# Performance work log

Measured on AMD Instinct MI355X. Metric: run time of the kernel, lower is better.

## Reference

```python
import jax, jax.numpy as jnp
import numpy as np

S, DIM, E, K = 16384, 4096, 64, 2

def setup_inputs() -> dict:
    key = jax.random.key(0)
    kx, kw = jax.random.split(key)
    x = jax.random.normal(kx, (S, DIM), dtype=jnp.float32)
    W = jax.random.normal(kw, (E, DIM), dtype=jnp.float32) * (1.0 / np.sqrt(DIM))
    b = jnp.zeros((E,), dtype=jnp.float32)
    return {"x": x, "W": W, "b": b}

def reference(x, W, b):
    # Router linear: [S, dim] @ [dim, E] + [E] -> [S, E]
    logits = jnp.einsum('sd,ed->se', x, W) + b
    probs = jax.nn.softmax(logits, axis=-1)              # [S, E]
    topk_vals, topk_idx = jax.lax.top_k(probs, K)        # [S, K], [S, K]
    # Load-balance aux loss (Switch Transformer style)
    importance = probs.mean(axis=0)                      # [E]
    hard1 = topk_idx[:, 0]                               # [S]
    load = jax.ops.segment_sum(jnp.ones((S,), dtype=probs.dtype), hard1,
                               num_segments=E) / max(S, 1)
    aux_loss = E * jnp.sum(importance * load)
    return (topk_idx, topk_vals, aux_loss)
```

## Files before the change

### kernel.cpp

```cpp
#include <hip/hip_runtime.h>
#include <hip/hip_bf16.h>

#define SROWS 16384
#define DIMK  4096
#define NE    64
#define BM    16
#define NBLK  (SROWS/BM)
#define NSTEP 16
#define WSPLIT_SHORTS 262144
#define WSOFF_F 262144
#define WSOFF2  (WSOFF_F + NBLK*64)

typedef __attribute__((ext_vector_type(8))) short short8;
typedef __attribute__((ext_vector_type(4))) float f32x4;

__device__ __forceinline__ void split8(const float4 a, const float4 c, short8& hi, short8& lo) {
    float f[8] = {a.x, a.y, a.z, a.w, c.x, c.y, c.z, c.w};
    #pragma unroll
    for (int i = 0; i < 8; ++i) {
        unsigned short h = __bfloat16_as_ushort(__float2bfloat16(f[i]));
        float hf = __uint_as_float((unsigned)h << 16);
        unsigned short l = __bfloat16_as_ushort(__float2bfloat16(f[i] - hf));
        hi[i] = (short)h;
        lo[i] = (short)l;
    }
}

__global__ void w_split(const float* __restrict__ W, unsigned short* __restrict__ wsp)
{
    const int idx   = blockIdx.x * 256 + threadIdx.x;
    const int kslot = idx & 511;
    const int e     = idx >> 9;
    const float* p = W + (size_t)e * DIMK + kslot * 8;
    float4 va = *reinterpret_cast<const float4*>(p);
    float4 vb = *reinterpret_cast<const float4*>(p + 4);
    short8 hi, lo;
    split8(va, vb, hi, lo);
    *reinterpret_cast<short8*>(wsp + (size_t)(kslot * 64 + e) * 8)                 = hi;
    *reinterpret_cast<short8*>(wsp + WSPLIT_SHORTS + (size_t)(kslot * 64 + e) * 8) = lo;
}

__device__ __forceinline__ void gl_lds16(const void* g, void* l) {
    __builtin_amdgcn_global_load_lds(
        (const __attribute__((address_space(1))) void*)g,
        (__attribute__((address_space(3))) void*)l, 16, 0, 0);
}

__global__ __launch_bounds__(256, 4) void gate_main(
    const float* __restrict__ x, const unsigned short* __restrict__ wsp,
    const float* __restrict__ b, float* __restrict__ out, float* __restrict__ ws)
{
    __shared__ __align__(16) char smem[32768];

    const int tid  = threadIdx.x;
    const int lane = tid & 63;
    const int ksw  = __builtin_amdgcn_readfirstlane(tid >> 6);
    const int row0 = blockIdx.x * BM;

    const float* xsq[4];
    #pragma unroll
    for (int q = 0; q < 4; ++q) {
        const int r = ksw * 4 + q;
        xsq[q] = x + (size_t)(row0 + r) * DIMK + ((lane ^ (r & 7)) * 4);
    }

    auto STAGE = [&](int st, int bsel) {
        char* xb = smem + bsel * 16384;
        #pragma unroll
        for (int q = 0; q < 4; ++q)
            gl_lds16(xsq[q] + (size_t)st * 256, xb + (ksw * 4 + q) * 1024 + lane * 16);
    };

    f32x4 acc[4];
    #pragma unroll
    for (int n = 0; n < 4; ++n) acc[n] = (f32x4){0.f, 0.f, 0.f, 0.f};

    const int rm = lane & 7;
    const char* xrow = smem + (lane & 15) * 1024;

    STAGE(0, 0);

    #pragma unroll 1
    for (int st = 0; st < NSTEP; ++st) {
        asm volatile("s_waitcnt vmcnt(0)" ::: "memory");
        __builtin_amdgcn_s_barrier();
        __builtin_amdgcn_sched_barrier(0);
        if (st + 1 < NSTEP) STAGE(st + 1, (st + 1) & 1);

        const char* xb = xrow + (st & 1) * 16384;

        #pragma unroll
        for (int c2 = 0; c2 < 2; ++c2) {
            const int ga = ksw * 16 + c2 * 8 + 2 * (lane >> 4);
            float4 xa = *reinterpret_cast<const float4*>(xb + ((ga    ) ^ rm) * 16);
            float4 xc = *reinterpret_cast<const float4*>(xb + ((ga + 1) ^ rm) * 16);
            short8 ah, al;
            split8(xa, xc, ah, al);

            const int ksl = st * 32 + ksw * 8 + c2 * 4 + (lane >> 4);
            const unsigned short* bp = wsp + ((size_t)ksl * 64 + (lane & 15)) * 8;
            short8 bh[4], bl[4];
            #pragma unroll
            for (int n = 0; n < 4; ++n) {
                bh[n] = *reinterpret_cast<const short8*>(bp + n * 128);
                bl[n] = *reinterpret_cast<const short8*>(bp + WSPLIT_SHORTS + n * 128);
            }

            #pragma unroll
            for (int n = 0; n < 4; ++n)
                acc[n] = __builtin_amdgcn_mfma_f32_16x16x32_bf16(ah, bh[n], acc[n], 0, 0, 0);
            #pragma unroll
            for (int n = 0; n < 4; ++n)
                acc[n] = __builtin_amdgcn_mfma_f32_16x16x32_bf16(ah, bl[n], acc[n], 0, 0, 0);
            #pragma unroll
            for (int n = 0; n < 4; ++n)
                acc[n] = __builtin_amdgcn_mfma_f32_16x16x32_bf16(al, bh[n], acc[n], 0, 0, 0);
        }
    }

    __syncthreads();

    float* const part = reinterpret_cast<float*>(smem);
    float* const Lb   = reinterpret_cast<float*>(smem + 12288);
    float* const red  = reinterpret_cast<float*>(smem + 17792);

    if (ksw > 0) {
        #pragma unroll
        for (int n = 0; n < 4; ++n)
            #pragma unroll
            for (int j = 0; j < 4; ++j)
                part[(ksw - 1) * 1024 + lane * 16 + n * 4 + j] = acc[n][j];
    }
    __syncthreads();
    if (ksw == 0) {
        #pragma unroll
        for (int n = 0; n < 4; ++n) {
            #pragma unroll
            for (int j = 0; j < 4; ++j) {
                float v = acc[n][j]
                        + part[0 * 1024 + lane * 16 + n * 4 + j]
                        + part[1 * 1024 + lane * 16 + n * 4 + j]
                        + part[2 * 1024 + lane * 16 + n * 4 + j];
                const int e  = n * 16 + (lane & 15);
                const int rl = (lane >> 4) * 4 + j;
                Lb[e * 17 + rl] = v;
            }
        }
    }
    __syncthreads();

    float impAcc = 0.f, cntAcc = 0.f;
    const float blane = b[lane];
    float* outIdx = out;
    float* outVal = out + (size_t)SROWS * 2;

    #pragma unroll 1
    for (int rr = 0; rr < 4; ++rr) {
        const int r = ksw * 4 + rr;
        const float logit = Lb[lane * 17 + r] + blane;

        float v1 = logit; int i1 = lane;
        #pragma unroll
        for (int off = 32; off; off >>= 1) {
            float ov = __shfl_xor(v1, off);
            int   oi = __shfl_xor(i1, off);
            if (ov > v1 || (ov == v1 && oi < i1)) { v1 = ov; i1 = oi; }
        }
        float p = expf(logit - v1);
        float ssum = p;
        #pragma unroll
        for (int off = 32; off; off >>= 1) ssum += __shfl_xor(ssum, off);

        float v2 = (lane == i1) ? -3.402823466e38f : logit;
        int i2 = lane;
        #pragma unroll
        for (int off = 32; off; off >>= 1) {
            float ov = __shfl_xor(v2, off);
            int   oi = __shfl_xor(i2, off);
            if (ov > v2 || (ov == v2 && oi < i2)) { v2 = ov; i2 = oi; }
        }

        impAcc += p / ssum;
        cntAcc += (i1 == lane) ? 1.f : 0.f;

        if (lane == 0) {
            const int sr = row0 + r;
            outIdx[sr * 2 + 0] = (float)i1;
            outIdx[sr * 2 + 1] = (float)i2;
            outVal[sr * 2 + 0] = 1.f / ssum;
            outVal[sr * 2 + 1] = expf(v2 - v1) / ssum;
        }
    }

    __syncthreads();
    red[ksw * 64 + lane]       = impAcc;
    red[256 + ksw * 64 + lane] = cntAcc;
    __syncthreads();
    if (tid < 64) {
        float si = 0.f, sc2 = 0.f;
        #pragma unroll
        for (int g = 0; g < 4; ++g) {
            si  += red[g * 64 + tid];
            sc2 += red[256 + g * 64 + tid];
        }
        ws[WSOFF_F + (size_t)blockIdx.x * 64 + tid] = si;
        ws[WSOFF2  + (size_t)blockIdx.x * 64 + tid] = sc2;
    }
}

__global__ void gate_reduce(const float* __restrict__ ws, float* __restrict__ out)
{
    __shared__ float li[64 * 64], lc[64 * 64];
    const int t = threadIdx.x;
    const int g  = t >> 4;
    const int e4 = (t & 15) * 4;
    float4 si = make_float4(0.f, 0.f, 0.f, 0.f);
    float4 sc = make_float4(0.f, 0.f, 0.f, 0.f);
    const int base = g * 16;
    #pragma unroll 4
    for (int bb = base; bb < base + 16; ++bb) {
        float4 a = *reinterpret_cast<const float4*>(&ws[WSOFF_F + (size_t)bb * 64 + e4]);
        float4 c = *reinterpret_cast<const float4*>(&ws[WSOFF2  + (size_t)bb * 64 + e4]);
        si.x += a.x; si.y += a.y; si.z += a.z; si.w += a.w;
        sc.x += c.x; sc.y += c.y; sc.z += c.z; sc.w += c.w;
    }
    *reinterpret_cast<float4*>(&li[g * 64 + e4]) = si;
    *reinterpret_cast<float4*>(&lc[g * 64 + e4]) = sc;
    __syncthreads();
    if (t < 64) {
        float ti = 0.f, tc = 0.f;
        #pragma unroll 8
        for (int gg = 0; gg < 64; ++gg) { ti += li[gg * 64 + t]; tc += lc[gg * 64 + t]; }
        li[t] = ti * tc;
    }
    __syncthreads();
    if (t == 0) {
        float s = 0.f;
        for (int i = 0; i < NE; ++i) s += li[i];
        out[(size_t)SROWS * 4] = s * ((float)NE / ((float)SROWS * (float)SROWS));
    }
}

extern "C" void kernel_launch(void* const* d_in, const int* in_sizes, int n_in,
                              void* d_out, int out_size, void* d_ws, size_t ws_size,
                              hipStream_t stream)
{
    const float* x = (const float*)d_in[0];
    const float* W = (const float*)d_in[1];
    const float* b = (const float*)d_in[2];
    float* out = (float*)d_out;
    unsigned short* wsp = (unsigned short*)d_ws;
    float* wsf = (float*)d_ws;

    w_split<<<128, 256, 0, stream>>>(W, wsp);
    gate_main<<<NBLK, 256, 0, stream>>>(x, wsp, b, out, wsf);
    gate_reduce<<<1, 1024, 0, stream>>>(wsf, out);
}
```

Before: 89.47 us.

## Use 16 waves per block with wider split-K and dynamic LDS

```diff
diff --git a/kernel.cpp b/kernel.cpp
--- a/kernel.cpp
+++ b/kernel.cpp
@@ -6,10 +6,11 @@
 #define NE    64
 #define BM    16
 #define NBLK  (SROWS/BM)
-#define NSTEP 16
+#define NSTEP 8
 #define WSPLIT_SHORTS 262144
 #define WSOFF_F 262144
 #define WSOFF2  (WSOFF_F + NBLK*64)
+#define LDS_BYTES 98304
 
 typedef __attribute__((ext_vector_type(8))) short short8;
 typedef __attribute__((ext_vector_type(4))) float f32x4;
@@ -46,29 +47,24 @@
         (__attribute__((address_space(3))) void*)l, 16, 0, 0);
 }
 
-__global__ __launch_bounds__(256, 4) void gate_main(
+__global__ __launch_bounds__(1024, 4) void gate_main(
     const float* __restrict__ x, const unsigned short* __restrict__ wsp,
     const float* __restrict__ b, float* __restrict__ out, float* __restrict__ ws)
 {
-    __shared__ __align__(16) char smem[32768];
+    extern __shared__ __align__(16) char smem[];
 
     const int tid  = threadIdx.x;
     const int lane = tid & 63;
-    const int ksw  = __builtin_amdgcn_readfirstlane(tid >> 6);
+    const int wid  = __builtin_amdgcn_readfirstlane(tid >> 6);
     const int row0 = blockIdx.x * BM;
 
-    const float* xsq[4];
-    #pragma unroll
-    for (int q = 0; q < 4; ++q) {
-        const int r = ksw * 4 + q;
-        xsq[q] = x + (size_t)(row0 + r) * DIMK + ((lane ^ (r & 7)) * 4);
-    }
+    const float* xs0 = x + (size_t)(row0 + wid) * DIMK + (lane ^ (wid & 7)) * 4;
+    const float* xs1 = xs0 + 256;
 
     auto STAGE = [&](int st, int bsel) {
-        char* xb = smem + bsel * 16384;
-        #pragma unroll
-        for (int q = 0; q < 4; ++q)
-            gl_lds16(xsq[q] + (size_t)st * 256, xb + (ksw * 4 + q) * 1024 + lane * 16);
+        char* xb = smem + bsel * 32768 + wid * 2048;
+        gl_lds16(xs0 + (size_t)st * 512, xb + lane * 16);
+        gl_lds16(xs1 + (size_t)st * 512, xb + 1024 + lane * 16);
     };
 
     f32x4 acc[4];
@@ -76,71 +72,72 @@
     for (int n = 0; n < 4; ++n) acc[n] = (f32x4){0.f, 0.f, 0.f, 0.f};
 
     const int rm = lane & 7;
-    const char* xrow = smem + (lane & 15) * 1024;
+    const char* xrow = smem + (lane & 15) * 2048;
+    const int ga = wid * 8 + 2 * (lane >> 4);
 
     STAGE(0, 0);
+    asm volatile("s_waitcnt vmcnt(0)" ::: "memory");
+    __builtin_amdgcn_s_barrier();
+    __builtin_amdgcn_sched_barrier(0);
 
     #pragma unroll 1
     for (int st = 0; st < NSTEP; ++st) {
+        if (st + 1 < NSTEP) STAGE(st + 1, (st + 1) & 1);
+        __builtin_amdgcn_sched_barrier(0);
+
+        const char* xb = xrow + (st & 1) * 32768;
+        float4 xa = *reinterpret_cast<const float4*>(xb + ((ga    ) ^ rm) * 16);
+        float4 xc = *reinterpret_cast<const float4*>(xb + ((ga + 1) ^ rm) * 16);
+        short8 ah, al;
+        split8(xa, xc, ah, al);
+
+        const int ksl = st * 64 + wid * 4 + (lane >> 4);
+        const unsigned short* bp = wsp + ((size_t)ksl * 64 + (lane & 15)) * 8;
+        short8 bh[4], bl[4];
+        #pragma unroll
+        for (int n = 0; n < 4; ++n) {
+            bh[n] = *reinterpret_cast<const short8*>(bp + n * 128);
+            bl[n] = *reinterpret_cast<const short8*>(bp + WSPLIT_SHORTS + n * 128);
+        }
+
+        #pragma unroll
+        for (int n = 0; n < 4; ++n)
+            acc[n] = __builtin_amdgcn_mfma_f32_16x16x32_bf16(ah, bh[n], acc[n], 0, 0, 0);
+        #pragma unroll
+        for (int n = 0; n < 4; ++n)
+            acc[n] = __builtin_amdgcn_mfma_f32_16x16x32_bf16(ah, bl[n], acc[n], 0, 0, 0);
+        #pragma unroll
+        for (int n = 0; n < 4; ++n)
+            acc[n] = __builtin_amdgcn_mfma_f32_16x16x32_bf16(al, bh[n], acc[n], 0, 0, 0);
+
         asm volatile("s_waitcnt vmcnt(0)" ::: "memory");
         __builtin_amdgcn_s_barrier();
         __builtin_amdgcn_sched_barrier(0);
-        if (st + 1 < NSTEP) STAGE(st + 1, (st + 1) & 1);
-
-        const char* xb = xrow + (st & 1) * 16384;
-
-        #pragma unroll
-        for (int c2 = 0; c2 < 2; ++c2) {
-            const int ga = ksw * 16 + c2 * 8 + 2 * (lane >> 4);
-            float4 xa = *reinterpret_cast<const float4*>(xb + ((ga    ) ^ rm) * 16);
-            float4 xc = *reinterpret_cast<const float4*>(xb + ((ga + 1) ^ rm) * 16);
-            short8 ah, al;
-            split8(xa, xc, ah, al);
-
-            const int ksl = st * 32 + ksw * 8 + c2 * 4 + (lane >> 4);
-            const unsigned short* bp = wsp + ((size_t)ksl * 64 + (lane & 15)) * 8;
-            short8 bh[4], bl[4];
-            #pragma unroll
-            for (int n = 0; n < 4; ++n) {
-                bh[n] = *reinterpret_cast<const short8*>(bp + n * 128);
-                bl[n] = *reinterpret_cast<const short8*>(bp + WSPLIT_SHORTS + n * 128);
-            }
-
-            #pragma unroll
-            for (int n = 0; n < 4; ++n)
-                acc[n] = __builtin_amdgcn_mfma_f32_16x16x32_bf16(ah, bh[n], acc[n], 0, 0, 0);
-            #pragma unroll
-            for (int n = 0; n < 4; ++n)
-                acc[n] = __builtin_amdgcn_mfma_f32_16x16x32_bf16(ah, bl[n], acc[n], 0, 0, 0);
-            #pragma unroll
-            for (int n = 0; n < 4; ++n)
-                acc[n] = __builtin_amdgcn_mfma_f32_16x16x32_bf16(al, bh[n], acc[n], 0, 0, 0);
-        }
     }
 
     __syncthreads();
 
     float* const part = reinterpret_cast<float*>(smem);
-    float* const Lb   = reinterpret_cast<float*>(smem + 12288);
-    float* const red  = reinterpret_cast<float*>(smem + 17792);
-
-    if (ksw > 0) {
+    float* const Lb   = reinterpret_cast<float*>(smem + 61440);
+    float* const red  = reinterpret_cast<float*>(smem + 65792);
+
+    if (wid > 0) {
         #pragma unroll
         for (int n = 0; n < 4; ++n)
             #pragma unroll
             for (int j = 0; j < 4; ++j)
-                part[(ksw - 1) * 1024 + lane * 16 + n * 4 + j] = acc[n][j];
-    }
-    __syncthreads();
-    if (ksw == 0) {
+                part[(wid - 1) * 1024 + lane * 16 + n * 4 + j] = acc[n][j];
+    }
+    __syncthreads();
+    if (wid == 0) {
         #pragma unroll
         for (int n = 0; n < 4; ++n) {
             #pragma unroll
             for (int j = 0; j < 4; ++j) {
-                float v = acc[n][j]
-                        + part[0 * 1024 + lane * 16 + n * 4 + j]
-                        + part[1 * 1024 + lane * 16 + n * 4 + j]
-                        + part[2 * 1024 + lane * 16 + n * 4 + j];
+                float v = acc[n][j];
+                #pragma unroll
+                for (int g = 0; g < 15; ++g)
+                    v += part[g * 1024 + lane * 16 + n * 4 + j];
                 const int e  = n * 16 + (lane & 15);
                 const int rl = (lane >> 4) * 4 + j;
                 Lb[e * 17 + rl] = v;
@@ -149,59 +146,55 @@
     }
     __syncthreads();
 
-    float impAcc = 0.f, cntAcc = 0.f;
     const float blane = b[lane];
     float* outIdx = out;
     float* outVal = out + (size_t)SROWS * 2;
 
-    #pragma unroll 1
-    for (int rr = 0; rr < 4; ++rr) {
-        const int r = ksw * 4 + rr;
-        const float logit = Lb[lane * 17 + r] + blane;
-
-        float v1 = logit; int i1 = lane;
-        #pragma unroll
-        for (int off = 32; off; off >>= 1) {
-            float ov = __shfl_xor(v1, off);
-            int   oi = __shfl_xor(i1, off);
-            if (ov > v1 || (ov == v1 && oi < i1)) { v1 = ov; i1 = oi; }
-        }
-        float p = expf(logit - v1);
-        float ssum = p;
-        #pragma unroll
-        for (int off = 32; off; off >>= 1) ssum += __shfl_xor(ssum, off);
-
-        float v2 = (lane == i1) ? -3.402823466e38f : logit;
-        int i2 = lane;
-        #pragma unroll
-        for (int off = 32; off; off >>= 1) {
-            float ov = __shfl_xor(v2, off);
-            int   oi = __shfl_xor(i2, off);
-            if (ov > v2 || (ov == v2 && oi < i2)) { v2 = ov; i2 = oi; }
-        }
-
-        impAcc += p / ssum;
-        cntAcc += (i1 == lane) ? 1.f : 0.f;
-
-        if (lane == 0) {
-            const int sr = row0 + r;
-            outIdx[sr * 2 + 0] = (float)i1;
-            outIdx[sr * 2 + 1] = (float)i2;
-            outVal[sr * 2 + 0] = 1.f / ssum;
-            outVal[sr * 2 + 1] = expf(v2 - v1) / ssum;
-        }
-    }
-
-    __syncthreads();
-    red[ksw * 64 + lane]       = impAcc;
-    red[256 + ksw * 64 + lane] = cntAcc;
+    const int r = wid;
+    const float logit = Lb[lane * 17 + r] + blane;
+
+    float v1 = logit; int i1 = lane;
+    #pragma unroll
+    for (int off = 32; off; off >>= 1) {
+        float ov = __shfl_xor(v1, off);
+        int   oi = __shfl_xor(i1, off);
+        if (ov > v1 || (ov == v1 && oi < i1)) { v1 = ov; i1 = oi; }
+    }
+    float p = expf(logit - v1);
+    float ssum = p;
+    #pragma unroll
+    for (int off = 32; off; off >>= 1) ssum += __shfl_xor(ssum, off);
+
+    float v2 = (lane == i1) ? -3.402823466e38f : logit;
+    int i2 = lane;
+    #pragma unroll
+    for (int off = 32; off; off >>= 1) {
+        float ov = __shfl_xor(v2, off);
+        int   oi = __shfl_xor(i2, off);
+        if (ov > v2 || (ov == v2 && oi < i2)) { v2 = ov; i2 = oi; }
+    }
+
+    const float impAcc = p / ssum;
+    const float cntAcc = (i1 == lane) ? 1.f : 0.f;
+
+    if (lane == 0) {
+        const int sr = row0 + r;
+        outIdx[sr * 2 + 0] = (float)i1;
+        outIdx[sr * 2 + 1] = (float)i2;
+        outVal[sr * 2 + 0] = 1.f / ssum;
+        outVal[sr * 2 + 1] = expf(v2 - v1) / ssum;
+    }
+
+    __syncthreads();
+    red[wid * 64 + lane]        = impAcc;
+    red[1024 + wid * 64 + lane] = cntAcc;
     __syncthreads();
     if (tid < 64) {
         float si = 0.f, sc2 = 0.f;
         #pragma unroll
-        for (int g = 0; g < 4; ++g) {
+        for (int g = 0; g < 16; ++g) {
             si  += red[g * 64 + tid];
-            sc2 += red[256 + g * 64 + tid];
+            sc2 += red[1024 + g * 64 + tid];
         }
         ws[WSOFF_F + (size_t)blockIdx.x * 64 + tid] = si;
         ws[WSOFF2  + (size_t)blockIdx.x * 64 + tid] = sc2;
@@ -252,7 +245,10 @@
     unsigned short* wsp = (unsigned short*)d_ws;
     float* wsf = (float*)d_ws;
 
+    hipFuncSetAttribute(reinterpret_cast<const void*>(gate_main),
+                        hipFuncAttributeMaxDynamicSharedMemorySize, LDS_BYTES);
+
     w_split<<<128, 256, 0, stream>>>(W, wsp);
-    gate_main<<<NBLK, 256, 0, stream>>>(x, wsp, b, out, wsf);
+    gate_main<<<NBLK, 1024, LDS_BYTES, stream>>>(x, wsp, b, out, wsf);
     gate_reduce<<<1, 1024, 0, stream>>>(wsf, out);
 }
```

Result: slower. 142.7 us (+59.4%).

## Split K across eight private-slab waves to remove per-step block barriers

Applied to the files above, without the earlier changes.

```diff
diff --git a/kernel.cpp b/kernel.cpp
--- a/kernel.cpp
+++ b/kernel.cpp
@@ -6,7 +6,10 @@
 #define NE    64
 #define BM    16
 #define NBLK  (SROWS/BM)
+#define KSPL  8
+#define KSEG  (DIMK/KSPL)
 #define NSTEP 16
+#define SBK   32
 #define WSPLIT_SHORTS 262144
 #define WSOFF_F 262144
 #define WSOFF2  (WSOFF_F + NBLK*64)
@@ -46,7 +49,7 @@
         (__attribute__((address_space(3))) void*)l, 16, 0, 0);
 }
 
-__global__ __launch_bounds__(256, 4) void gate_main(
+__global__ __launch_bounds__(512, 6) void gate_main(
     const float* __restrict__ x, const unsigned short* __restrict__ wsp,
     const float* __restrict__ b, float* __restrict__ out, float* __restrict__ ws)
 {
@@ -54,21 +57,24 @@
 
     const int tid  = threadIdx.x;
     const int lane = tid & 63;
-    const int ksw  = __builtin_amdgcn_readfirstlane(tid >> 6);
+    const int wid  = __builtin_amdgcn_readfirstlane(tid >> 6);
     const int row0 = blockIdx.x * BM;
 
-    const float* xsq[4];
+    const float* xsq[2];
     #pragma unroll
-    for (int q = 0; q < 4; ++q) {
-        const int r = ksw * 4 + q;
-        xsq[q] = x + (size_t)(row0 + r) * DIMK + ((lane ^ (r & 7)) * 4);
-    }
+    for (int q = 0; q < 2; ++q) {
+        const int s = q * 64 + lane;
+        const int r = s >> 3;
+        const int glog = (s & 7) ^ (r & 7);
+        xsq[q] = x + (size_t)(row0 + r) * DIMK + wid * KSEG + glog * 4;
+    }
+    char* const xslab = smem + wid * 4096;
 
     auto STAGE = [&](int st, int bsel) {
-        char* xb = smem + bsel * 16384;
-        #pragma unroll
-        for (int q = 0; q < 4; ++q)
-            gl_lds16(xsq[q] + (size_t)st * 256, xb + (ksw * 4 + q) * 1024 + lane * 16);
+        char* xb = xslab + bsel * 2048;
+        #pragma unroll
+        for (int q = 0; q < 2; ++q)
+            gl_lds16(xsq[q] + (size_t)st * SBK, xb + q * 1024 + lane * 16);
     };
 
     f32x4 acc[4];
@@ -76,74 +82,81 @@
     for (int n = 0; n < 4; ++n) acc[n] = (f32x4){0.f, 0.f, 0.f, 0.f};
 
     const int rm = lane & 7;
-    const char* xrow = smem + (lane & 15) * 1024;
+    const char* xrow = xslab + (lane & 15) * 128;
+    const int h = lane >> 4;
 
     STAGE(0, 0);
 
     #pragma unroll 1
     for (int st = 0; st < NSTEP; ++st) {
         asm volatile("s_waitcnt vmcnt(0)" ::: "memory");
-        __builtin_amdgcn_s_barrier();
         __builtin_amdgcn_sched_barrier(0);
         if (st + 1 < NSTEP) STAGE(st + 1, (st + 1) & 1);
 
-        const char* xb = xrow + (st & 1) * 16384;
-
-        #pragma unroll
-        for (int c2 = 0; c2 < 2; ++c2) {
-            const int ga = ksw * 16 + c2 * 8 + 2 * (lane >> 4);
-            float4 xa = *reinterpret_cast<const float4*>(xb + ((ga    ) ^ rm) * 16);
-            float4 xc = *reinterpret_cast<const float4*>(xb + ((ga + 1) ^ rm) * 16);
-            short8 ah, al;
-            split8(xa, xc, ah, al);
-
-            const int ksl = st * 32 + ksw * 8 + c2 * 4 + (lane >> 4);
-            const unsigned short* bp = wsp + ((size_t)ksl * 64 + (lane & 15)) * 8;
-            short8 bh[4], bl[4];
-            #pragma unroll
-            for (int n = 0; n < 4; ++n) {
-                bh[n] = *reinterpret_cast<const short8*>(bp + n * 128);
-                bl[n] = *reinterpret_cast<const short8*>(bp + WSPLIT_SHORTS + n * 128);
-            }
-
-            #pragma unroll
-            for (int n = 0; n < 4; ++n)
-                acc[n] = __builtin_amdgcn_mfma_f32_16x16x32_bf16(ah, bh[n], acc[n], 0, 0, 0);
-            #pragma unroll
-            for (int n = 0; n < 4; ++n)
-                acc[n] = __builtin_amdgcn_mfma_f32_16x16x32_bf16(ah, bl[n], acc[n], 0, 0, 0);
-            #pragma unroll
-            for (int n = 0; n < 4; ++n)
-                acc[n] = __builtin_amdgcn_mfma_f32_16x16x32_bf16(al, bh[n], acc[n], 0, 0, 0);
-        }
+        const char* xb = xrow + (st & 1) * 2048;
+        float4 xa = *reinterpret_cast<const float4*>(xb + ((2 * h    ) ^ rm) * 16);
+        float4 xc = *reinterpret_cast<const float4*>(xb + ((2 * h + 1) ^ rm) * 16);
+        short8 ah, al;
+        split8(xa, xc, ah, al);
+
+        const int ksl = wid * 64 + st * 4 + h;
+        const unsigned short* bp = wsp + ((size_t)ksl * 64 + (lane & 15)) * 8;
+        short8 bh[4], bl[4];
+        #pragma unroll
+        for (int n = 0; n < 4; ++n) {
+            bh[n] = *reinterpret_cast<const short8*>(bp + n * 128);
+            bl[n] = *reinterpret_cast<const short8*>(bp + WSPLIT_SHORTS + n * 128);
+        }
+
+        #pragma unroll
+        for (int n = 0; n < 4; ++n)
+            acc[n] = __builtin_amdgcn_mfma_f32_16x16x32_bf16(ah, bh[n], acc[n], 0, 0, 0);
+        #pragma unroll
+        for (int n = 0; n < 4; ++n)
+            acc[n] = __builtin_amdgcn_mfma_f32_16x16x32_bf16(ah, bl[n], acc[n], 0, 0, 0);
+        #pragma unroll
+        for (int n = 0; n < 4; ++n)
+            acc[n] = __builtin_amdgcn_mfma_f32_16x16x32_bf16(al, bh[n], acc[n], 0, 0, 0);
     }
 
     __syncthreads();
 
     float* const part = reinterpret_cast<float*>(smem);
-    float* const Lb   = reinterpret_cast<float*>(smem + 12288);
-    float* const red  = reinterpret_cast<float*>(smem + 17792);
-
-    if (ksw > 0) {
+
+    if (wid > 0) {
         #pragma unroll
         for (int n = 0; n < 4; ++n)
             #pragma unroll
             for (int j = 0; j < 4; ++j)
-                part[(ksw - 1) * 1024 + lane * 16 + n * 4 + j] = acc[n][j];
-    }
-    __syncthreads();
-    if (ksw == 0) {
+                part[(wid - 1) * 1088 + lane * 17 + n * 4 + j] = acc[n][j];
+    }
+    __syncthreads();
+    if (wid == 0) {
         #pragma unroll
         for (int n = 0; n < 4; ++n) {
             #pragma unroll
             for (int j = 0; j < 4; ++j) {
-                float v = acc[n][j]
-                        + part[0 * 1024 + lane * 16 + n * 4 + j]
-                        + part[1 * 1024 + lane * 16 + n * 4 + j]
-                        + part[2 * 1024 + lane * 16 + n * 4 + j];
+                float v = acc[n][j];
+                #pragma unroll
+                for (int g = 0; g < 7; ++g)
+                    v += part[g * 1088 + lane * 17 + n * 4 + j];
+                acc[n][j] = v;
+            }
+        }
+    }
+    __syncthreads();
+
+    float* const Lb  = reinterpret_cast<float*>(smem);
+    float* const red = reinterpret_cast<float*>(smem + 8192);
+
+    if (wid == 0) {
+        #pragma unroll
+        for (int n = 0; n < 4; ++n) {
+            #pragma unroll
+            for (int j = 0; j < 4; ++j) {
                 const int e  = n * 16 + (lane & 15);
                 const int rl = (lane >> 4) * 4 + j;
-                Lb[e * 17 + rl] = v;
+                Lb[e * 17 + rl] = acc[n][j];
             }
         }
     }
@@ -155,8 +168,8 @@
     float* outVal = out + (size_t)SROWS * 2;
 
     #pragma unroll 1
-    for (int rr = 0; rr < 4; ++rr) {
-        const int r = ksw * 4 + rr;
+    for (int rr = 0; rr < 2; ++rr) {
+        const int r = wid * 2 + rr;
         const float logit = Lb[lane * 17 + r] + blane;
 
         float v1 = logit; int i1 = lane;
@@ -193,15 +206,15 @@
     }
 
     __syncthreads();
-    red[ksw * 64 + lane]       = impAcc;
-    red[256 + ksw * 64 + lane] = cntAcc;
+    red[wid * 64 + lane]       = impAcc;
+    red[512 + wid * 64 + lane] = cntAcc;
     __syncthreads();
     if (tid < 64) {
         float si = 0.f, sc2 = 0.f;
         #pragma unroll
-        for (int g = 0; g < 4; ++g) {
+        for (int g = 0; g < KSPL; ++g) {
             si  += red[g * 64 + tid];
-            sc2 += red[256 + g * 64 + tid];
+            sc2 += red[512 + g * 64 + tid];
         }
         ws[WSOFF_F + (size_t)blockIdx.x * 64 + tid] = si;
         ws[WSOFF2  + (size_t)blockIdx.x * 64 + tid] = sc2;
@@ -253,6 +266,6 @@
     float* wsf = (float*)d_ws;
 
     w_split<<<128, 256, 0, stream>>>(W, wsp);
-    gate_main<<<NBLK, 256, 0, stream>>>(x, wsp, b, out, wsf);
+    gate_main<<<NBLK, 512, 0, stream>>>(x, wsp, b, out, wsf);
     gate_reduce<<<1, 1024, 0, stream>>>(wsf, out);
 }
```

After: 85.17 us. 1.05x faster.
